# Kernel optimization log

Hardware: AMD Instinct MI355X
Metric: run time of the kernel (lower is better)

Reference implementation:

```python
import jax, jax.numpy as jnp
import numpy as np
import math

N_OFFSETS = 72
FMAP_H = 10
FMAP_W = 25
IMG_W = 800
STRIDE = 32


def _gen_anchor(start, angle_deg, ys):
    # anchor layout: [score0, score1, start_y(1-sy), start_x, length, xs...]
    a = np.zeros(5 + len(ys), np.float32)
    ang = math.radians(angle_deg)
    sx, sy = start
    a[2] = 1.0 - sy
    a[3] = sx
    a[5:] = (sx + (1.0 - ys - 1.0 + sy) / math.tan(ang)) * IMG_W
    return a


def _side(angles, nb, x=None, y=None):
    if x is None:
        starts = [(xx, 1.0) for xx in np.linspace(1.0, 0.0, nb)]
    else:
        starts = [(x, yy) for yy in np.linspace(1.0, 0.0, nb)]
    ys_full = np.linspace(1.0, 0.0, N_OFFSETS)
    ys_cut = np.linspace(1.0, 0.0, FMAP_H)
    A = np.stack([_gen_anchor(s, a, ys_full) for s in starts for a in angles])
    Ac = np.stack([_gen_anchor(s, a, ys_cut) for s in starts for a in angles])
    return A, Ac


def _build_anchors():
    left = _side([72., 60., 49., 39., 30., 22.], 72, x=0.0)
    right = _side([108., 120., 131., 141., 150., 158.], 72, x=1.0)
    bottom = _side([165., 150., 141., 131., 120., 108., 100., 90., 80., 72., 60., 49., 39., 30., 15.], 128, y=1.0)
    anchors = np.concatenate([left[0], bottom[0], right[0]]).astype(np.float32)  # (N, 5+72)
    cut = np.concatenate([left[1], bottom[1], right[1]])                          # (N, 5+Hf)
    unclamped = np.flip(np.round(cut[:, 5:] / STRIDE), axis=1).astype(np.int32)   # (N, Hf)
    cut_xs = np.clip(unclamped, 0, FMAP_W - 1).astype(np.int32)
    invalid = (unclamped < 0) | (unclamped > FMAP_W)
    return anchors, cut_xs, invalid


def setup_inputs() -> dict:
    key = jax.random.key(0)
    ks = jax.random.split(key, 10)
    B, C_IN, CF = 8, 512, 64
    anchors_np, cut_xs_np, invalid_np = _build_anchors()
    N = anchors_np.shape[0]  # 2784
    D = CF * FMAP_H          # 640
    s = 0.01
    return {
        "x": jax.random.normal(ks[0], (B, C_IN, FMAP_H, FMAP_W), jnp.float32),
        "conv_w": jax.random.normal(ks[1], (CF, C_IN), jnp.float32) * s,
        "conv_b": jnp.zeros((CF,), jnp.float32),
        "attn_w": jax.random.normal(ks[2], (N - 1, D), jnp.float32) * s,
        "attn_b": jnp.zeros((N - 1,), jnp.float32),
        "cls_w": jax.random.normal(ks[3], (2, 2 * D), jnp.float32) * s,
        "cls_b": jnp.zeros((2,), jnp.float32),
        "reg_w": jax.random.normal(ks[4], (N_OFFSETS + 1, 2 * D), jnp.float32) * s,
        "reg_b": jnp.zeros((N_OFFSETS + 1,), jnp.float32),
        "anchors": jnp.asarray(anchors_np),
        "cut_xs": jnp.asarray(cut_xs_np),
        "invalid_mask": jnp.asarray(invalid_np),
    }


def reference(x, conv_w, conv_b, attn_w, attn_b, cls_w, cls_b, reg_w, reg_b, anchors, cut_xs, invalid_mask):
    B = x.shape[0]
    N, Hf = cut_xs.shape
    Cf = conv_w.shape[0]
    # 1x1 conv
    feat = jnp.einsum('bchw,fc->bfhw', x, conv_w) + conv_b[None, :, None, None]
    # cut anchor features: gather irregular (v,u) columns -> (B, Cf, N, Hf)
    ys = jnp.arange(Hf)
    g = feat[:, :, ys[None, :], cut_xs]
    g = jnp.where(invalid_mask[None, None], jnp.zeros((), x.dtype), g)
    pf = g.transpose(0, 2, 1, 3).reshape(B, N, Cf * Hf)  # (B, N, D)
    # learned attention over anchors
    scores = jnp.einsum('bnd,md->bnm', pf, attn_w) + attn_b  # (B, N, N-1)
    attn = jax.nn.softmax(scores, axis=-1)
    # scatter into NxN matrix with zero diagonal (row i gets its N-1 values in off-diag cols)
    rows = jnp.arange(N)[:, None]
    cols = jnp.arange(N - 1)[None, :] + (jnp.arange(N - 1)[None, :] >= rows)
    attn_mat = jnp.zeros((B, N, N), x.dtype).at[:, rows, cols].set(attn)
    # aggregate features across anchors
    att_feats = jnp.einsum('bij,bjd->bid', attn_mat, pf)
    cat = jnp.concatenate([att_feats, pf], axis=-1)  # (B, N, 2D)
    cls_logits = jnp.einsum('bnd,cd->bnc', cat, cls_w) + cls_b
    reg = jnp.einsum('bnd,cd->bnc', cat, reg_w) + reg_b  # (B, N, n_offsets+1)
    lanes = jnp.broadcast_to(anchors[None], (B,) + anchors.shape)
    lanes = lanes.at[:, :, 4].set(reg[:, :, 0])
    lanes = lanes.at[:, :, 5:].add(reg[:, :, 1:])
    return cls_logits, lanes, attn_mat
```

## Files before the change

### kernel.cpp

```cpp
#include <hip/hip_runtime.h>
#include <hip/hip_fp8.h>

typedef unsigned short ushort_t;
typedef unsigned char  uchar_t;
typedef unsigned int   uint32;
typedef __attribute__((ext_vector_type(8))) short short8;
typedef __attribute__((ext_vector_type(4))) float f32x4;
typedef __attribute__((ext_vector_type(4))) uint32 u32x4;
typedef long fp8x8;

#define B_     8
#define CIN    512
#define HFM    10
#define WFM    25
#define CF     64
#define NANCH  2784
#define NANCHP 2816
#define NM     2783
#define NMPAD  2816
#define D_     640
#define D2     1280
#define ALEN   77
#define M_     (B_*NANCH)
#define NO     128

#define VMCNT(N)   asm volatile("s_waitcnt vmcnt(" #N ")" ::: "memory")
#define S_BARRIER() do { __builtin_amdgcn_s_barrier(); __builtin_amdgcn_sched_barrier(0); } while (0)

__device__ __forceinline__ ushort_t f2bf(float f) {
    uint32 u = __float_as_uint(f);
    u += 0x7fffu + ((u >> 16) & 1u);
    return (ushort_t)(u >> 16);
}
__device__ __forceinline__ float bf2f(ushort_t h) {
    return __uint_as_float(((uint32)h) << 16);
}
__device__ __forceinline__ uchar_t f2fp8(float f) {
    __hip_fp8_e4m3 h(f);
    return (uchar_t)h.__x;
}

__device__ __forceinline__ void gload16(const ushort_t* g, ushort_t* l) {
    __builtin_amdgcn_global_load_lds(
        (const __attribute__((address_space(1))) void*)g,
        (__attribute__((address_space(3))) void*)l, 16, 0, 0);
}
__device__ __forceinline__ void gload16b(const uchar_t* g, uchar_t* l) {
    __builtin_amdgcn_global_load_lds(
        (const __attribute__((address_space(1))) void*)g,
        (__attribute__((address_space(3))) void*)l, 16, 0, 0);
}

__global__ __launch_bounds__(256) void conv_feat_k(const float* __restrict__ x,
    const float* __restrict__ w, const float* __restrict__ bias,
    float* __restrict__ feat)
{
    int t = blockIdx.x * 256 + threadIdx.x;
    if (t >= B_ * CF * HFM * WFM) return;
    int pos = t % (HFM * WFM);
    int f   = (t / (HFM * WFM)) % CF;
    int b   = t / (CF * HFM * WFM);
    const float* xp = x + (size_t)b * CIN * HFM * WFM + pos;
    const float* wp = w + (size_t)f * CIN;
    float s = bias[f];
#pragma unroll 4
    for (int c = 0; c < CIN; ++c)
        s += xp[(size_t)c * (HFM * WFM)] * wp[c];
    feat[t] = s;
}

__global__ __launch_bounds__(256) void gather_pf_k(const float* __restrict__ feat,
    const int* __restrict__ cut_xs, const unsigned char* __restrict__ invalid,
    ushort_t* __restrict__ pf16, uchar_t* __restrict__ pf8)
{
    long long t = (long long)blockIdx.x * 256 + threadIdx.x;
    if (t >= (long long)M_ * D_) return;
    int d = (int)(t % D_);
    int r = (int)(t / D_);
    int n = r % NANCH;
    int b = r / NANCH;
    int f = d / HFM, h = d - f * HFM;
    int idx = n * HFM + h;
    float v = 0.f;
    if (!invalid[idx]) {
        int xs = cut_xs[idx];
        v = feat[((size_t)(b * CF + f) * HFM + h) * WFM + xs];
    }
    pf16[t] = f2bf(v);
    pf8[t]  = f2fp8(v * 4.f);
}

#define PREP_N1 (NMPAD * D_)
#define PREP_N2 (128 * D2)
#define PREP_N3 (B_ * NO * 32)
#define PREP_N4 (M_ * 17)
#define PREP_TOT (PREP_N1 + PREP_N2 + PREP_N3 + PREP_N4)

__global__ __launch_bounds__(256) void prep_all_k(
    const float* __restrict__ attn_w, const float* __restrict__ cls_w,
    const float* __restrict__ reg_w,
    uchar_t* __restrict__ aw8, ushort_t* __restrict__ hw16,
    ushort_t* __restrict__ Gt, ushort_t* __restrict__ E)
{
    int t = blockIdx.x * 256 + threadIdx.x;
    if (t < PREP_N1) {
        int m = t / D_;
        aw8[t] = (m < NM) ? f2fp8(attn_w[(size_t)m * D_ + (t % D_)] * 32.f) : (uchar_t)0;
        return;
    }
    t -= PREP_N1;
    if (t < PREP_N2) {
        int o = t / D2, k = t % D2;
        float v = 0.f;
        if (o < 2)       v = cls_w[(size_t)o * D2 + k];
        else if (o < 75) v = reg_w[(size_t)(o - 2) * D2 + k];
        hw16[t] = (o < 75) ? f2bf(v) : (ushort_t)0;
        return;
    }
    t -= PREP_N2;
    if (t < PREP_N3) {
        int n = t & 31, o = (t >> 5) & (NO - 1), b = t >> 12;
        Gt[((size_t)b * NO + o) * NANCHP + NANCH + n] = 0;
        return;
    }
    t -= PREP_N3;
    if (t < M_) {
        E[(size_t)t * NANCHP + (t % NANCH)] = 0;
    } else {
        int idx = t - M_;
        int r = idx >> 4, w = idx & 15;
        *(uint32*)&E[(size_t)r * NANCHP + NANCH + 2 * w] = 0;
    }
}

__global__ __launch_bounds__(256, 4) void scores_mfma_k(
    const uchar_t* __restrict__ A8,
    const uchar_t* __restrict__ B8,
    const float* __restrict__ attn_b,
    ushort_t* __restrict__ E)
{
    __shared__ __align__(16) uchar_t As[2][8192];
    __shared__ __align__(16) uchar_t Bs[2][8192];
    const int orig = blockIdx.x;
    const int xcd = orig & 7, pos = orig >> 3;
    const int start = (xcd < 4) ? xcd * 479 : 1916 + (xcd - 4) * 478;
    const int idx = start + pos;
    const int rowb = idx / 22, colb = idx - rowb * 22;
    const int row0 = rowb * 128, col0 = colb * 128;
    const int t = threadIdx.x;
    const int wid = t >> 6, lane = t & 63;
    const int wr = wid >> 1, wc = wid & 1;
    const int srow = lane >> 2;
    const int swku = (((lane & 3) ^ ((lane >> 3) & 3)) * 16);
    const uchar_t* gA = A8 + (size_t)(row0 + wid * 32 + srow) * D_ + swku;
    const uchar_t* gB = B8 + (size_t)(col0 + wid * 32 + srow) * D_ + swku;
    f32x4 acc[4][4];
#pragma unroll
    for (int i = 0; i < 4; ++i)
#pragma unroll
        for (int j = 0; j < 4; ++j) acc[i][j] = (f32x4){0.f, 0.f, 0.f, 0.f};
    const int cl = lane & 15, q = lane >> 4;
    const int cv = (cl >> 1) & 3;

    auto STAGE = [&](int buf, int k0) {
        uchar_t* la = &As[buf][wid * 2048];
        uchar_t* lb = &Bs[buf][wid * 2048];
        gload16b(gA + k0, la);
        gload16b(gA + k0 + 16 * D_, la + 1024);
        gload16b(gB + k0, lb);
        gload16b(gB + k0 + 16 * D_, lb + 1024);
    };
    auto COMPUTE = [&](int buf) {
#pragma unroll
        for (int ks = 0; ks < 2; ++ks) {
            const int c = ks * 4 + q;
            const int co8 = (((c >> 1) ^ cv) * 16) + ((c & 1) * 8);
            fp8x8 af[4], bv[4];
#pragma unroll
            for (int i = 0; i < 4; ++i)
                af[i] = *(const fp8x8*)&As[buf][(wr * 64 + i * 16 + cl) * 64 + co8];
#pragma unroll
            for (int j = 0; j < 4; ++j)
                bv[j] = *(const fp8x8*)&Bs[buf][(wc * 64 + j * 16 + cl) * 64 + co8];
            __builtin_amdgcn_s_setprio(1);
#pragma unroll
            for (int i = 0; i < 4; ++i)
#pragma unroll
                for (int j = 0; j < 4; ++j)
                    acc[i][j] = __builtin_amdgcn_mfma_f32_16x16x32_fp8_fp8(af[i], bv[j], acc[i][j], 0, 0, 0);
            __builtin_amdgcn_s_setprio(0);
        }
    };

    const int NT = D_ / 64;
    STAGE(0, 0); STAGE(1, 64);
    int cur = 0;
    for (int tl = 0; tl < NT - 1; ++tl) {
        VMCNT(4); S_BARRIER();
        COMPUTE(cur);
        S_BARRIER();
        if (tl + 2 < NT) STAGE(cur, (tl + 2) * 64);
        cur ^= 1;
    }
    VMCNT(0); S_BARRIER();
    COMPUTE(cur);

    const float inv_sc = 1.0f / 128.0f;
#pragma unroll
    for (int i = 0; i < 4; ++i) {
#pragma unroll
        for (int ee = 0; ee < 4; ++ee) {
            int r = row0 + wr * 64 + i * 16 + q * 4 + ee;
            int n = r % NANCH;
            ushort_t* orow = E + (size_t)r * NANCHP;
#pragma unroll
            for (int j = 0; j < 4; ++j) {
                int m = col0 + wc * 64 + j * 16 + cl;
                if (m < NM) orow[m + (m >= n)] = f2bf(__expf(acc[i][j][ee] * inv_sc + attn_b[m]));
            }
        }
    }
}

__global__ __launch_bounds__(256) void normalize_k(const ushort_t* __restrict__ E,
    float* __restrict__ attn, float* __restrict__ rsum)
{
    const int r = blockIdx.x;
    float* row = attn + (size_t)r * NANCH;
    const ushort_t* row16 = E + (size_t)r * NANCHP;
    const int t = threadIdx.x;
    __shared__ float red[4];
    float vals[16];
    float s = 0.f;
#pragma unroll
    for (int i = 0; i < 2; ++i) {
        int c = t + i * 256;
        float v0 = 0.f, v1 = 0.f, v2 = 0.f, v3 = 0.f, v4 = 0.f, v5 = 0.f, v6 = 0.f, v7 = 0.f;
        if (c < 348) {
            u32x4 u = *(const u32x4*)&row16[8 * c];
            v0 = bf2f((ushort_t)(u.x & 0xffffu)); v1 = bf2f((ushort_t)(u.x >> 16));
            v2 = bf2f((ushort_t)(u.y & 0xffffu)); v3 = bf2f((ushort_t)(u.y >> 16));
            v4 = bf2f((ushort_t)(u.z & 0xffffu)); v5 = bf2f((ushort_t)(u.z >> 16));
            v6 = bf2f((ushort_t)(u.w & 0xffffu)); v7 = bf2f((ushort_t)(u.w >> 16));
        }
        vals[8 * i + 0] = v0; vals[8 * i + 1] = v1; vals[8 * i + 2] = v2; vals[8 * i + 3] = v3;
        vals[8 * i + 4] = v4; vals[8 * i + 5] = v5; vals[8 * i + 6] = v6; vals[8 * i + 7] = v7;
        s += ((v0 + v1) + (v2 + v3)) + ((v4 + v5) + (v6 + v7));
    }
    for (int off = 32; off; off >>= 1) s += __shfl_down(s, off);
    if ((t & 63) == 0) red[t >> 6] = s;
    __syncthreads();
    s = red[0] + red[1] + red[2] + red[3];
    float inv = 1.0f / s;
    if (t == 0) rsum[r] = s;
#pragma unroll
    for (int i = 0; i < 2; ++i) {
        int c = t + i * 256;
        if (c < 348) {
            float4 w0 = make_float4(vals[8 * i] * inv, vals[8 * i + 1] * inv,
                                    vals[8 * i + 2] * inv, vals[8 * i + 3] * inv);
            float4 w1 = make_float4(vals[8 * i + 4] * inv, vals[8 * i + 5] * inv,
                                    vals[8 * i + 6] * inv, vals[8 * i + 7] * inv);
            *(float4*)&row[8 * c]     = w0;
            *(float4*)&row[8 * c + 4] = w1;
        }
    }
}

__global__ __launch_bounds__(256, 2) void gx_mfma_k(
    const ushort_t* __restrict__ A,
    const ushort_t* __restrict__ W,
    ushort_t* __restrict__ Gt)
{
    __shared__ __align__(16) ushort_t As[2][8192];
    __shared__ __align__(16) ushort_t Bs[2][8192];
    const int t = threadIdx.x;
    const int wid = t >> 6, lane = t & 63;
    const int wr = wid >> 1, wc = wid & 1;
    const int row0 = blockIdx.x * 128;
    const int r8 = lane >> 3;
    const int ck = (lane & 7) ^ r8;
    const ushort_t* gA = A + (size_t)(row0 + wid * 8 + r8) * D_ + ck * 8;
    const ushort_t* gB = W + (size_t)(wid * 8 + r8) * D2 + ck * 8;
    f32x4 acc[4][4];
#pragma unroll
    for (int i = 0; i < 4; ++i)
#pragma unroll
        for (int j = 0; j < 4; ++j) acc[i][j] = (f32x4){0.f, 0.f, 0.f, 0.f};
    const int cl = lane & 15, q = lane >> 4, cl7 = lane & 7;

    auto STAGE = [&](int buf, int k0) {
        ushort_t* la = &As[buf][wid * 512];
        ushort_t* lb = &Bs[buf][wid * 512];
#pragma unroll
        for (int j = 0; j < 4; ++j) {
            gload16(gA + k0 + (size_t)j * 32 * D_, la + j * 2048);
            gload16(gB + k0 + (size_t)j * 32 * D2, lb + j * 2048);
        }
    };
    auto COMPUTE = [&](int buf) {
#pragma unroll
        for (int ks = 0; ks < 2; ++ks) {
            short8 af[4], bv[4];
            const int co = ((ks * 4 + q) ^ cl7) * 8;
#pragma unroll
            for (int i = 0; i < 4; ++i)
                af[i] = *(const short8*)&As[buf][(wr * 64 + i * 16 + cl) * 64 + co];
#pragma unroll
            for (int j = 0; j < 4; ++j)
                bv[j] = *(const short8*)&Bs[buf][(wc * 64 + j * 16 + cl) * 64 + co];
            __builtin_amdgcn_s_setprio(1);
#pragma unroll
            for (int i = 0; i < 4; ++i)
#pragma unroll
                for (int j = 0; j < 4; ++j)
                    acc[i][j] = __builtin_amdgcn_mfma_f32_16x16x32_bf16(af[i], bv[j], acc[i][j], 0, 0, 0);
            __builtin_amdgcn_s_setprio(0);
        }
    };

    const int NT = D_ / 64;
    STAGE(0, 0); STAGE(1, 64);
    int cur = 0;
    for (int tl = 0; tl < NT - 1; ++tl) {
        VMCNT(8); S_BARRIER();
        COMPUTE(cur);
        S_BARRIER();
        if (tl + 2 < NT) STAGE(cur, (tl + 2) * 64);
        cur ^= 1;
    }
    VMCNT(0); S_BARRIER();
    COMPUTE(cur);

#pragma unroll
    for (int i = 0; i < 4; ++i) {
#pragma unroll
        for (int ee = 0; ee < 4; ++ee) {
            int r = row0 + wr * 64 + i * 16 + q * 4 + ee;
            int b = r / NANCH, nl = r - b * NANCH;
#pragma unroll
            for (int j = 0; j < 4; ++j) {
                int o = wc * 64 + j * 16 + cl;
                Gt[((size_t)b * NO + o) * NANCHP + nl] = f2bf(acc[i][j][ee]);
            }
        }
    }
}

__global__ __launch_bounds__(256, 4) void final_mfma_k(
    const ushort_t* __restrict__ E16,
    const ushort_t* __restrict__ pf16,
    const ushort_t* __restrict__ Gt,
    const ushort_t* __restrict__ W,
    float* __restrict__ part)
{
    __shared__ __align__(16) ushort_t As[2][4096];
    __shared__ __align__(16) ushort_t Bs[2][4096];
    const int b = blockIdx.x & 7;
    const int u = blockIdx.x >> 3;
    const int rb = u % 22, kc = u / 22;
    const int g0 = (kc < 4) ? kc * 22 : 88;
    const int NT = (kc < 4) ? 22 : 20;
    const int t = threadIdx.x;
    const int wid = t >> 6, lane = t & 63;
    const int wr = wid >> 1, wc = wid & 1;
    const int srow = lane >> 2;
    const int swk  = (((lane & 3) ^ ((lane >> 3) & 3)) * 8);
    const size_t arow = (size_t)b * NANCH + rb * 128 + wid * 32 + srow;
    const ushort_t* gAa = E16  + arow * NANCHP + swk;
    const ushort_t* gAp = pf16 + arow * D_ + swk;
    const ushort_t* gBg = Gt + ((size_t)b * NO + wid * 32 + srow) * NANCHP + swk;
    const ushort_t* gBw = W + (size_t)(wid * 32 + srow) * D2 + D_ + swk;
    f32x4 acc[4][4];
#pragma unroll
    for (int i = 0; i < 4; ++i)
#pragma unroll
        for (int j = 0; j < 4; ++j) acc[i][j] = (f32x4){0.f, 0.f, 0.f, 0.f};
    const int cl = lane & 15, q = lane >> 4;
    const int ra = wr * 64 + cl, rbb = wc * 64 + cl;
    const int aoff = ra * 32 + ((q ^ ((ra >> 1) & 3)) * 8);
    const int boff = rbb * 32 + ((q ^ ((rbb >> 1) & 3)) * 8);

    auto STAGE = [&](int buf, int gt) {
        ushort_t* la = &As[buf][wid * 1024];
        ushort_t* lb = &Bs[buf][wid * 1024];
        if (gt < 88) {
            const int k0 = gt * 32;
            gload16(gAa + k0, la);
            gload16(gAa + k0 + (size_t)16 * NANCHP, la + 512);
            gload16(gBg + k0, lb);
            gload16(gBg + k0 + (size_t)16 * NANCHP, lb + 512);
        } else {
            const int kk = (gt - 88) * 32;
            gload16(gAp + kk, la);
            gload16(gAp + kk + (size_t)16 * D_, la + 512);
            gload16(gBw + kk, lb);
            gload16(gBw + kk + (size_t)16 * D2, lb + 512);
        }
    };
    auto COMPUTE = [&](int buf) {
        short8 af[4], bv[4];
#pragma unroll
        for (int i = 0; i < 4; ++i) af[i] = *(const short8*)&As[buf][aoff + i * 512];
#pragma unroll
        for (int j = 0; j < 4; ++j) bv[j] = *(const short8*)&Bs[buf][boff + j * 512];
        __builtin_amdgcn_s_setprio(1);
#pragma unroll
        for (int i = 0; i < 4; ++i)
#pragma unroll
            for (int j = 0; j < 4; ++j)
                acc[i][j] = __builtin_amdgcn_mfma_f32_16x16x32_bf16(af[i], bv[j], acc[i][j], 0, 0, 0);
        __builtin_amdgcn_s_setprio(0);
    };

    STAGE(0, g0); STAGE(1, g0 + 1);
    int cur = 0;
    for (int tl = 0; tl < NT - 1; ++tl) {
        VMCNT(4); S_BARRIER();
        COMPUTE(cur);
        S_BARRIER();
        if (tl + 2 < NT) STAGE(cur, g0 + tl + 2);
        cur ^= 1;
    }
    VMCNT(0); S_BARRIER();
    COMPUTE(cur);

    float* pout = part + (size_t)kc * M_ * NO;
#pragma unroll
    for (int i = 0; i < 4; ++i) {
#pragma unroll
        for (int ee = 0; ee < 4; ++ee) {
            int nl = rb * 128 + wr * 64 + i * 16 + q * 4 + ee;
            if (nl < NANCH) {
                int r = b * NANCH + nl;
#pragma unroll
                for (int j = 0; j < 4; ++j) {
                    int oo = wc * 64 + j * 16 + cl;
                    pout[(size_t)r * NO + oo] = acc[i][j][ee];
                }
            }
        }
    }
}

__global__ __launch_bounds__(256) void reduce_heads_k(
    const float* __restrict__ part,
    const float* __restrict__ rsum,
    const float* __restrict__ cls_b, const float* __restrict__ reg_b,
    const float* __restrict__ anchors,
    float* __restrict__ cls_out, float* __restrict__ lanes)
{
    int t = blockIdx.x * 256 + threadIdx.x;
    if (t >= M_ * 80) return;
    int r = t / 80, oo = t - r * 80;
    int nl = r % NANCH;
    if (oo < 75) {
        float inv = 1.0f / rsum[r];
        size_t base = (size_t)r * NO + oo, st = (size_t)M_ * NO;
        float v = ((part[base] + part[base + st]) + (part[base + 2 * st] + part[base + 3 * st])) * inv
                + part[base + 4 * st];
        if (oo < 2) {
            cls_out[(size_t)r * 2 + oo] = v + cls_b[oo];
        } else {
            int qq = oo - 2;
            int c = 4 + qq;
            float res = v + reg_b[qq];
            if (qq > 0) res += anchors[(size_t)nl * ALEN + c];
            lanes[(size_t)r * ALEN + c] = res;
        }
    } else if (oo < 79) {
        int c = oo - 75;
        lanes[(size_t)r * ALEN + c] = anchors[(size_t)nl * ALEN + c];
    }
}

extern "C" void kernel_launch(void* const* d_in, const int* in_sizes, int n_in,
                              void* d_out, int out_size, void* d_ws, size_t ws_size,
                              hipStream_t stream)
{
    (void)in_sizes; (void)n_in; (void)out_size; (void)ws_size;
    const float* x       = (const float*)d_in[0];
    const float* conv_w  = (const float*)d_in[1];
    const float* conv_b  = (const float*)d_in[2];
    const float* attn_w  = (const float*)d_in[3];
    const float* attn_b  = (const float*)d_in[4];
    const float* cls_w   = (const float*)d_in[5];
    const float* cls_b   = (const float*)d_in[6];
    const float* reg_w   = (const float*)d_in[7];
    const float* reg_b   = (const float*)d_in[8];
    const float* anchors = (const float*)d_in[9];
    const int*   cut_xs  = (const int*)d_in[10];
    const unsigned char* invalid = (const unsigned char*)d_in[11];

    float* out     = (float*)d_out;
    float* cls_out = out;
    float* lanes   = out + (size_t)M_ * 2;
    float* attn    = out + (size_t)M_ * 2 + (size_t)M_ * ALEN;

    char* w = (char*)d_ws;
    float* feat      = (float*)w;    w += (size_t)B_ * CF * HFM * WFM * 4;
    ushort_t* pf16   = (ushort_t*)w; w += (size_t)M_ * D_ * 2;
    uchar_t* pf8     = (uchar_t*)w;  w += (size_t)M_ * D_;
    uchar_t* aw8     = (uchar_t*)w;  w += (size_t)NMPAD * D_;
    ushort_t* hw16   = (ushort_t*)w; w += (size_t)128 * D2 * 2;
    ushort_t* Gt     = (ushort_t*)w; w += (size_t)B_ * NO * NANCHP * 2;
    float* part      = (float*)w;    w += (size_t)5 * M_ * NO * 4;
    float* rsum      = (float*)w;    w += (size_t)M_ * 4;
    ushort_t* E16    = (ushort_t*)w; w += (size_t)(M_ + 32) * NANCHP * 2;

    conv_feat_k<<<(B_ * CF * HFM * WFM + 255) / 256, 256, 0, stream>>>(x, conv_w, conv_b, feat);
    gather_pf_k<<<(int)(((long long)M_ * D_ + 255) / 256), 256, 0, stream>>>(feat, cut_xs, invalid, pf16, pf8);
    prep_all_k<<<(PREP_TOT + 255) / 256, 256, 0, stream>>>(attn_w, cls_w, reg_w,
                                                           aw8, hw16, Gt, E16);

    gx_mfma_k<<<M_ / 128, 256, 0, stream>>>(pf16, hw16, Gt);

    scores_mfma_k<<<dim3(174 * 22), 256, 0, stream>>>(pf8, aw8, attn_b, E16);
    normalize_k<<<M_, 256, 0, stream>>>(E16, attn, rsum);

    final_mfma_k<<<dim3(5 * 22 * B_), 256, 0, stream>>>(E16, pf16, Gt, hw16, part);
    reduce_heads_k<<<(M_ * 80 + 255) / 256, 256, 0, stream>>>(part, rsum, cls_b, reg_b,
                                                              anchors, cls_out, lanes);
}
```

Measured before the change: 374.8 us.

## Store unnormalized attention and head projections in fp8 and use fp8 MFMA for aggregation

Switches the intermediate exp-score matrix E and the projected-heads matrix G from bf16 to fp8 e4m3 with fixed scale factors (16x and 64x), halving their memory traffic. The final aggregation over anchors now uses fp8 16x16x32 MFMA with 64-wide k tiles, split into four k-chunks plus two bf16 chunks for the pf·W term, so the grid grows from five to six partial slices. The normalize kernel reads fp8 rows with fewer threads, and the reduction compensates for the scales. This trades accuracy (fp8 softmax numerators and head projections) for less bandwidth and faster matrix math.

```diff
diff --git a/kernel.cpp b/kernel.cpp
--- a/kernel.cpp
+++ b/kernel.cpp
@@ -39,6 +39,9 @@
     __hip_fp8_e4m3 h(f);
     return (uchar_t)h.__x;
 }
+__device__ __forceinline__ float fp82f(uint32 b) {
+    __hip_fp8_e4m3 h; h.__x = (uchar_t)b; return (float)h;
+}
 
 __device__ __forceinline__ void gload16(const ushort_t* g, ushort_t* l) {
     __builtin_amdgcn_global_load_lds(
@@ -93,14 +96,14 @@
 #define PREP_N1 (NMPAD * D_)
 #define PREP_N2 (128 * D2)
 #define PREP_N3 (B_ * NO * 32)
-#define PREP_N4 (M_ * 17)
+#define PREP_N4 (M_ * 9)
 #define PREP_TOT (PREP_N1 + PREP_N2 + PREP_N3 + PREP_N4)
 
 __global__ __launch_bounds__(256) void prep_all_k(
     const float* __restrict__ attn_w, const float* __restrict__ cls_w,
     const float* __restrict__ reg_w,
     uchar_t* __restrict__ aw8, ushort_t* __restrict__ hw16,
-    ushort_t* __restrict__ Gt, ushort_t* __restrict__ E)
+    uchar_t* __restrict__ G8, uchar_t* __restrict__ E8)
 {
     int t = blockIdx.x * 256 + threadIdx.x;
     if (t < PREP_N1) {
@@ -120,16 +123,16 @@
     t -= PREP_N2;
     if (t < PREP_N3) {
         int n = t & 31, o = (t >> 5) & (NO - 1), b = t >> 12;
-        Gt[((size_t)b * NO + o) * NANCHP + NANCH + n] = 0;
+        G8[((size_t)b * NO + o) * NANCHP + NANCH + n] = 0;
         return;
     }
     t -= PREP_N3;
     if (t < M_) {
-        E[(size_t)t * NANCHP + (t % NANCH)] = 0;
+        E8[(size_t)t * NANCHP + (t % NANCH)] = 0;
     } else {
         int idx = t - M_;
-        int r = idx >> 4, w = idx & 15;
-        *(uint32*)&E[(size_t)r * NANCHP + NANCH + 2 * w] = 0;
+        int r = idx >> 3, w = idx & 7;
+        *(uint32*)&E8[(size_t)r * NANCHP + NANCH + 4 * w] = 0;
     }
 }
 
@@ -137,7 +140,7 @@
     const uchar_t* __restrict__ A8,
     const uchar_t* __restrict__ B8,
     const float* __restrict__ attn_b,
-    ushort_t* __restrict__ E)
+    uchar_t* __restrict__ E8)
 {
     __shared__ __align__(16) uchar_t As[2][8192];
     __shared__ __align__(16) uchar_t Bs[2][8192];
@@ -212,40 +215,42 @@
         for (int ee = 0; ee < 4; ++ee) {
             int r = row0 + wr * 64 + i * 16 + q * 4 + ee;
             int n = r % NANCH;
-            ushort_t* orow = E + (size_t)r * NANCHP;
+            uchar_t* orow = E8 + (size_t)r * NANCHP;
 #pragma unroll
             for (int j = 0; j < 4; ++j) {
                 int m = col0 + wc * 64 + j * 16 + cl;
-                if (m < NM) orow[m + (m >= n)] = f2bf(__expf(acc[i][j][ee] * inv_sc + attn_b[m]));
+                if (m < NM)
+                    orow[m + (m >= n)] = f2fp8(__expf(acc[i][j][ee] * inv_sc + attn_b[m]) * 16.f);
             }
         }
     }
 }
 
-__global__ __launch_bounds__(256) void normalize_k(const ushort_t* __restrict__ E,
+__global__ __launch_bounds__(256) void normalize_k(const uchar_t* __restrict__ E8,
     float* __restrict__ attn, float* __restrict__ rsum)
 {
     const int r = blockIdx.x;
     float* row = attn + (size_t)r * NANCH;
-    const ushort_t* row16 = E + (size_t)r * NANCHP;
+    const uchar_t* row8 = E8 + (size_t)r * NANCHP;
     const int t = threadIdx.x;
     __shared__ float red[4];
     float vals[16];
     float s = 0.f;
-#pragma unroll
-    for (int i = 0; i < 2; ++i) {
-        int c = t + i * 256;
-        float v0 = 0.f, v1 = 0.f, v2 = 0.f, v3 = 0.f, v4 = 0.f, v5 = 0.f, v6 = 0.f, v7 = 0.f;
-        if (c < 348) {
-            u32x4 u = *(const u32x4*)&row16[8 * c];
-            v0 = bf2f((ushort_t)(u.x & 0xffffu)); v1 = bf2f((ushort_t)(u.x >> 16));
-            v2 = bf2f((ushort_t)(u.y & 0xffffu)); v3 = bf2f((ushort_t)(u.y >> 16));
-            v4 = bf2f((ushort_t)(u.z & 0xffffu)); v5 = bf2f((ushort_t)(u.z >> 16));
-            v6 = bf2f((ushort_t)(u.w & 0xffffu)); v7 = bf2f((ushort_t)(u.w >> 16));
-        }
-        vals[8 * i + 0] = v0; vals[8 * i + 1] = v1; vals[8 * i + 2] = v2; vals[8 * i + 3] = v3;
-        vals[8 * i + 4] = v4; vals[8 * i + 5] = v5; vals[8 * i + 6] = v6; vals[8 * i + 7] = v7;
-        s += ((v0 + v1) + (v2 + v3)) + ((v4 + v5) + (v6 + v7));
+    if (t < 174) {
+        u32x4 u = *(const u32x4*)&row8[16 * t];
+#pragma unroll
+        for (int k = 0; k < 4; ++k) {
+            uint32 w = (k == 0) ? u.x : (k == 1) ? u.y : (k == 2) ? u.z : u.w;
+            vals[4 * k + 0] = fp82f(w & 0xffu);
+            vals[4 * k + 1] = fp82f((w >> 8) & 0xffu);
+            vals[4 * k + 2] = fp82f((w >> 16) & 0xffu);
+            vals[4 * k + 3] = fp82f(w >> 24);
+        }
+#pragma unroll
+        for (int k = 0; k < 16; ++k) s += vals[k];
+    } else {
+#pragma unroll
+        for (int k = 0; k < 16; ++k) vals[k] = 0.f;
     }
     for (int off = 32; off; off >>= 1) s += __shfl_down(s, off);
     if ((t & 63) == 0) red[t >> 6] = s;
@@ -253,16 +258,12 @@
     s = red[0] + red[1] + red[2] + red[3];
     float inv = 1.0f / s;
     if (t == 0) rsum[r] = s;
-#pragma unroll
-    for (int i = 0; i < 2; ++i) {
-        int c = t + i * 256;
-        if (c < 348) {
-            float4 w0 = make_float4(vals[8 * i] * inv, vals[8 * i + 1] * inv,
-                                    vals[8 * i + 2] * inv, vals[8 * i + 3] * inv);
-            float4 w1 = make_float4(vals[8 * i + 4] * inv, vals[8 * i + 5] * inv,
-                                    vals[8 * i + 6] * inv, vals[8 * i + 7] * inv);
-            *(float4*)&row[8 * c]     = w0;
-            *(float4*)&row[8 * c + 4] = w1;
+    if (t < 174) {
+#pragma unroll
+        for (int k = 0; k < 4; ++k) {
+            float4 w0 = make_float4(vals[4 * k] * inv, vals[4 * k + 1] * inv,
+                                    vals[4 * k + 2] * inv, vals[4 * k + 3] * inv);
+            *(float4*)&row[16 * t + 4 * k] = w0;
         }
     }
 }
@@ -270,7 +271,7 @@
 __global__ __launch_bounds__(256, 2) void gx_mfma_k(
     const ushort_t* __restrict__ A,
     const ushort_t* __restrict__ W,
-    ushort_t* __restrict__ Gt)
+    uchar_t* __restrict__ G8)
 {
     __shared__ __align__(16) ushort_t As[2][8192];
     __shared__ __align__(16) ushort_t Bs[2][8192];
@@ -341,89 +342,130 @@
 #pragma unroll
             for (int j = 0; j < 4; ++j) {
                 int o = wc * 64 + j * 16 + cl;
-                Gt[((size_t)b * NO + o) * NANCHP + nl] = f2bf(acc[i][j][ee]);
+                G8[((size_t)b * NO + o) * NANCHP + nl] = f2fp8(acc[i][j][ee] * 64.f);
             }
         }
     }
 }
 
 __global__ __launch_bounds__(256, 4) void final_mfma_k(
-    const ushort_t* __restrict__ E16,
+    const uchar_t* __restrict__ E8,
     const ushort_t* __restrict__ pf16,
-    const ushort_t* __restrict__ Gt,
+    const uchar_t* __restrict__ G8,
     const ushort_t* __restrict__ W,
     float* __restrict__ part)
 {
-    __shared__ __align__(16) ushort_t As[2][4096];
-    __shared__ __align__(16) ushort_t Bs[2][4096];
+    __shared__ __align__(16) uchar_t As[2][8192];
+    __shared__ __align__(16) uchar_t Bs[2][8192];
     const int b = blockIdx.x & 7;
     const int u = blockIdx.x >> 3;
     const int rb = u % 22, kc = u / 22;
-    const int g0 = (kc < 4) ? kc * 22 : 88;
-    const int NT = (kc < 4) ? 22 : 20;
     const int t = threadIdx.x;
     const int wid = t >> 6, lane = t & 63;
     const int wr = wid >> 1, wc = wid & 1;
-    const int srow = lane >> 2;
-    const int swk  = (((lane & 3) ^ ((lane >> 3) & 3)) * 8);
-    const size_t arow = (size_t)b * NANCH + rb * 128 + wid * 32 + srow;
-    const ushort_t* gAa = E16  + arow * NANCHP + swk;
-    const ushort_t* gAp = pf16 + arow * D_ + swk;
-    const ushort_t* gBg = Gt + ((size_t)b * NO + wid * 32 + srow) * NANCHP + swk;
-    const ushort_t* gBw = W + (size_t)(wid * 32 + srow) * D2 + D_ + swk;
+    const int cl = lane & 15, q = lane >> 4;
     f32x4 acc[4][4];
 #pragma unroll
     for (int i = 0; i < 4; ++i)
 #pragma unroll
         for (int j = 0; j < 4; ++j) acc[i][j] = (f32x4){0.f, 0.f, 0.f, 0.f};
-    const int cl = lane & 15, q = lane >> 4;
-    const int ra = wr * 64 + cl, rbb = wc * 64 + cl;
-    const int aoff = ra * 32 + ((q ^ ((ra >> 1) & 3)) * 8);
-    const int boff = rbb * 32 + ((q ^ ((rbb >> 1) & 3)) * 8);
-
-    auto STAGE = [&](int buf, int gt) {
-        ushort_t* la = &As[buf][wid * 1024];
-        ushort_t* lb = &Bs[buf][wid * 1024];
-        if (gt < 88) {
-            const int k0 = gt * 32;
-            gload16(gAa + k0, la);
-            gload16(gAa + k0 + (size_t)16 * NANCHP, la + 512);
-            gload16(gBg + k0, lb);
-            gload16(gBg + k0 + (size_t)16 * NANCHP, lb + 512);
-        } else {
-            const int kk = (gt - 88) * 32;
+
+    if (kc < 4) {
+        const int srow = lane >> 2;
+        const int swku = (((lane & 3) ^ ((lane >> 3) & 3)) * 16);
+        const size_t arow = (size_t)b * NANCH + rb * 128 + wid * 32 + srow;
+        const uchar_t* gA = E8 + arow * NANCHP + swku;
+        const uchar_t* gB = G8 + ((size_t)b * NO + wid * 32 + srow) * NANCHP + swku;
+        const int cv = (cl >> 1) & 3;
+        auto STAGE = [&](int buf, int gt) {
+            const int k0 = gt * 64;
+            uchar_t* la = &As[buf][wid * 2048];
+            uchar_t* lb = &Bs[buf][wid * 2048];
+            gload16b(gA + k0, la);
+            gload16b(gA + k0 + (size_t)16 * NANCHP, la + 1024);
+            gload16b(gB + k0, lb);
+            gload16b(gB + k0 + (size_t)16 * NANCHP, lb + 1024);
+        };
+        auto COMPUTE = [&](int buf) {
+#pragma unroll
+            for (int ks = 0; ks < 2; ++ks) {
+                const int c = ks * 4 + q;
+                const int co8 = (((c >> 1) ^ cv) * 16) + ((c & 1) * 8);
+                fp8x8 af[4], bv[4];
+#pragma unroll
+                for (int i = 0; i < 4; ++i)
+                    af[i] = *(const fp8x8*)&As[buf][(wr * 64 + i * 16 + cl) * 64 + co8];
+#pragma unroll
+                for (int j = 0; j < 4; ++j)
+                    bv[j] = *(const fp8x8*)&Bs[buf][(wc * 64 + j * 16 + cl) * 64 + co8];
+                __builtin_amdgcn_s_setprio(1);
+#pragma unroll
+                for (int i = 0; i < 4; ++i)
+#pragma unroll
+                    for (int j = 0; j < 4; ++j)
+                        acc[i][j] = __builtin_amdgcn_mfma_f32_16x16x32_fp8_fp8(af[i], bv[j], acc[i][j], 0, 0, 0);
+                __builtin_amdgcn_s_setprio(0);
+            }
+        };
+        const int g0 = kc * 11, NT = 11;
+        STAGE(0, g0); STAGE(1, g0 + 1);
+        int cur = 0;
+        for (int tl = 0; tl < NT - 1; ++tl) {
+            VMCNT(4); S_BARRIER();
+            COMPUTE(cur);
+            S_BARRIER();
+            if (tl + 2 < NT) STAGE(cur, g0 + tl + 2);
+            cur ^= 1;
+        }
+        VMCNT(0); S_BARRIER();
+        COMPUTE(cur);
+    } else {
+        const int srow = lane >> 2;
+        const int swk  = (((lane & 3) ^ ((lane >> 3) & 3)) * 8);
+        const size_t arow = (size_t)b * NANCH + rb * 128 + wid * 32 + srow;
+        const ushort_t* gAp = pf16 + arow * D_ + swk;
+        const ushort_t* gBw = W + (size_t)(wid * 32 + srow) * D2 + D_ + swk;
+        const int ra = wr * 64 + cl, rbb = wc * 64 + cl;
+        const int aoff = ra * 32 + ((q ^ ((ra >> 1) & 3)) * 8);
+        const int boff = rbb * 32 + ((q ^ ((rbb >> 1) & 3)) * 8);
+        auto STAGE = [&](int buf, int gt) {
+            const int kk = gt * 32;
+            ushort_t* la = (ushort_t*)&As[buf][wid * 2048];
+            ushort_t* lb = (ushort_t*)&Bs[buf][wid * 2048];
             gload16(gAp + kk, la);
             gload16(gAp + kk + (size_t)16 * D_, la + 512);
             gload16(gBw + kk, lb);
             gload16(gBw + kk + (size_t)16 * D2, lb + 512);
-        }
-    };
-    auto COMPUTE = [&](int buf) {
-        short8 af[4], bv[4];
-#pragma unroll
-        for (int i = 0; i < 4; ++i) af[i] = *(const short8*)&As[buf][aoff + i * 512];
-#pragma unroll
-        for (int j = 0; j < 4; ++j) bv[j] = *(const short8*)&Bs[buf][boff + j * 512];
-        __builtin_amdgcn_s_setprio(1);
-#pragma unroll
-        for (int i = 0; i < 4; ++i)
-#pragma unroll
-            for (int j = 0; j < 4; ++j)
-                acc[i][j] = __builtin_amdgcn_mfma_f32_16x16x32_bf16(af[i], bv[j], acc[i][j], 0, 0, 0);
-        __builtin_amdgcn_s_setprio(0);
-    };
-
-    STAGE(0, g0); STAGE(1, g0 + 1);
-    int cur = 0;
-    for (int tl = 0; tl < NT - 1; ++tl) {
-        VMCNT(4); S_BARRIER();
+        };
+        auto COMPUTE = [&](int buf) {
+            const ushort_t* As16 = (const ushort_t*)As[buf];
+            const ushort_t* Bs16 = (const ushort_t*)Bs[buf];
+            short8 af[4], bv[4];
+#pragma unroll
+            for (int i = 0; i < 4; ++i) af[i] = *(const short8*)&As16[aoff + i * 512];
+#pragma unroll
+            for (int j = 0; j < 4; ++j) bv[j] = *(const short8*)&Bs16[boff + j * 512];
+            __builtin_amdgcn_s_setprio(1);
+#pragma unroll
+            for (int i = 0; i < 4; ++i)
+#pragma unroll
+                for (int j = 0; j < 4; ++j)
+                    acc[i][j] = __builtin_amdgcn_mfma_f32_16x16x32_bf16(af[i], bv[j], acc[i][j], 0, 0, 0);
+            __builtin_amdgcn_s_setprio(0);
+        };
+        const int g0 = (kc - 4) * 10, NT = 10;
+        STAGE(0, g0); STAGE(1, g0 + 1);
+        int cur = 0;
+        for (int tl = 0; tl < NT - 1; ++tl) {
+            VMCNT(4); S_BARRIER();
+            COMPUTE(cur);
+            S_BARRIER();
+            if (tl + 2 < NT) STAGE(cur, g0 + tl + 2);
+            cur ^= 1;
+        }
+        VMCNT(0); S_BARRIER();
         COMPUTE(cur);
-        S_BARRIER();
-        if (tl + 2 < NT) STAGE(cur, g0 + tl + 2);
-        cur ^= 1;
-    }
-    VMCNT(0); S_BARRIER();
-    COMPUTE(cur);
+    }
 
     float* pout = part + (size_t)kc * M_ * NO;
 #pragma unroll
@@ -455,10 +497,10 @@
     int r = t / 80, oo = t - r * 80;
     int nl = r % NANCH;
     if (oo < 75) {
-        float inv = 1.0f / rsum[r];
+        float inv = 1.0f / (64.0f * rsum[r]);
         size_t base = (size_t)r * NO + oo, st = (size_t)M_ * NO;
         float v = ((part[base] + part[base + st]) + (part[base + 2 * st] + part[base + 3 * st])) * inv
-                + part[base + 4 * st];
+                + part[base + 4 * st] + part[base + 5 * st];
         if (oo < 2) {
             cls_out[(size_t)r * 2 + oo] = v + cls_b[oo];
         } else {
@@ -503,22 +545,22 @@
     uchar_t* pf8     = (uchar_t*)w;  w += (size_t)M_ * D_;
     uchar_t* aw8     = (uchar_t*)w;  w += (size_t)NMPAD * D_;
     ushort_t* hw16   = (ushort_t*)w; w += (size_t)128 * D2 * 2;
-    ushort_t* Gt     = (ushort_t*)w; w += (size_t)B_ * NO * NANCHP * 2;
-    float* part      = (float*)w;    w += (size_t)5 * M_ * NO * 4;
+    uchar_t* G8      = (uchar_t*)w;  w += (size_t)B_ * NO * NANCHP;
+    float* part      = (float*)w;    w += (size_t)6 * M_ * NO * 4;
     float* rsum      = (float*)w;    w += (size_t)M_ * 4;
-    ushort_t* E16    = (ushort_t*)w; w += (size_t)(M_ + 32) * NANCHP * 2;
+    uchar_t* E8      = (uchar_t*)w;  w += (size_t)(M_ + 32) * NANCHP;
 
     conv_feat_k<<<(B_ * CF * HFM * WFM + 255) / 256, 256, 0, stream>>>(x, conv_w, conv_b, feat);
     gather_pf_k<<<(int)(((long long)M_ * D_ + 255) / 256), 256, 0, stream>>>(feat, cut_xs, invalid, pf16, pf8);
     prep_all_k<<<(PREP_TOT + 255) / 256, 256, 0, stream>>>(attn_w, cls_w, reg_w,
-                                                           aw8, hw16, Gt, E16);
-
-    gx_mfma_k<<<M_ / 128, 256, 0, stream>>>(pf16, hw16, Gt);
-
-    scores_mfma_k<<<dim3(174 * 22), 256, 0, stream>>>(pf8, aw8, attn_b, E16);
-    normalize_k<<<M_, 256, 0, stream>>>(E16, attn, rsum);
-
-    final_mfma_k<<<dim3(5 * 22 * B_), 256, 0, stream>>>(E16, pf16, Gt, hw16, part);
+                                                           aw8, hw16, G8, E8);
+
+    gx_mfma_k<<<M_ / 128, 256, 0, stream>>>(pf16, hw16, G8);
+
+    scores_mfma_k<<<dim3(174 * 22), 256, 0, stream>>>(pf8, aw8, attn_b, E8);
+    normalize_k<<<M_, 256, 0, stream>>>(E8, attn, rsum);
+
+    final_mfma_k<<<dim3(6 * 22 * B_), 256, 0, stream>>>(E8, pf16, G8, hw16, part);
     reduce_heads_k<<<(M_ * 80 + 255) / 256, 256, 0, stream>>>(part, rsum, cls_b, reg_b,
                                                               anchors, cls_out, lanes);
 }
```

Result: faster. 358.8 us (-4.3%).
